# Kernel optimization log

Hardware: AMD Instinct MI355X
Metric: run time of the kernel (lower is better)

Reference implementation:

```python
import jax, jax.numpy as jnp
import numpy as np

FONT_NUM = 190
HID = 256
HEADS = 2
EPS = 1e-5


def _bn(x, g, b, m, v):
    # eval-mode BatchNorm over the last (channel) axis
    return (x - m) * (g * jax.lax.rsqrt(v + EPS)) + b


def _gru(x, Wih, Whh, bih, bhh):
    # x: [B, S, D]; PyTorch gate order r, z, n. Returns all hidden states [B, S, H].
    B, S, _ = x.shape
    H = Whh.shape[1]
    xp = x @ Wih.T + bih  # [B, S, 3H] -- one big GEMM for all timesteps
    def step(h, xt):
        gh = h @ Whh.T + bhh
        xr, xz, xn = jnp.split(xt, 3, axis=-1)
        hr, hz, hn = jnp.split(gh, 3, axis=-1)
        r = jax.nn.sigmoid(xr + hr)
        z = jax.nn.sigmoid(xz + hz)
        n = jnp.tanh(xn + r * hn)
        h_new = (1.0 - z) * n + z * h
        return h_new, h_new
    h0 = jnp.zeros((B, H), x.dtype)
    _, hs = jax.lax.scan(step, h0, jnp.swapaxes(xp, 0, 1))
    return jnp.swapaxes(hs, 0, 1)


def _forward(img_emb, text_embs, len_mask, label_mask, labels,
             img_W, img_b, img_g, img_beta, img_m, img_v,
             g1_Wih, g1_Whh, g1_bih, g1_bhh, tl_W, tl_b,
             t_g, t_beta, t_m, t_v,
             g2_Wih, g2_Whh, g2_bih, g2_bhh, cl_W, cl_b,
             c_g, c_beta, c_m, c_v,
             attn_Win, attn_bin, attn_Wout, attn_bout, pred_W, pred_b):
    # img encoder: Linear -> BN -> (Dropout eval=id) -> ReLU
    img_fea = jax.nn.relu(_bn(img_emb @ img_W.T + img_b, img_g, img_beta, img_m, img_v))  # [B,H]
    # text encoder: GRU -> ReLU -> Linear, then BN+ReLU (torch does this in [B,C,S]; equivalent over channels)
    t = jax.nn.relu(_gru(text_embs, g1_Wih, g1_Whh, g1_bih, g1_bhh))
    t = t @ tl_W.T + tl_b
    text_fea = jax.nn.relu(_bn(t, t_g, t_beta, t_m, t_v))  # [B,S,H]
    len_info = len_mask.sum(axis=1)  # [B]
    # NOTE: sum over ALL timesteps divided by valid length (faithful to source)
    mean = text_fea.sum(axis=1) / len_info[:, None]  # [B,H]
    contrast = text_fea - mean[:, None, :]
    c = jax.nn.relu(_gru(contrast, g2_Wih, g2_Whh, g2_bih, g2_bhh))
    c = c @ cl_W.T + cl_b
    contrast_fea = jax.nn.relu(_bn(c, c_g, c_beta, c_m, c_v))  # [B,S,H]
    B, S, H = text_fea.shape
    hd = H // HEADS
    # batched 3-token self-attention: collapse the per-timestep python loop into one call
    tokens = jnp.stack([
        jnp.broadcast_to(img_fea[:, None, :], (B, S, H)), text_fea, contrast_fea
    ], axis=0).reshape(3, B * S, H)  # [3, N, H]
    Wq, Wk, Wv = jnp.split(attn_Win, 3, axis=0)
    bq, bk, bv = jnp.split(attn_bin, 3, axis=0)
    scale = 1.0 / jnp.sqrt(jnp.asarray(hd, tokens.dtype))
    q = (tokens @ Wq.T + bq).reshape(3, B * S, HEADS, hd) * scale
    k = (tokens @ Wk.T + bk).reshape(3, B * S, HEADS, hd)
    v = (tokens @ Wv.T + bv).reshape(3, B * S, HEADS, hd)
    scores = jnp.einsum('tnhd,snhd->nhts', q, k)  # [N, heads, 3, 3]
    attn = jax.nn.softmax(scores, axis=-1)
    o = jnp.einsum('nhts,snhd->tnhd', attn, v).reshape(3, B * S, H)
    o = o @ attn_Wout.T + attn_bout
    last = o.mean(axis=0).reshape(B, S, H)  # att_fea.mean(0) over the 3 tokens
    logits = last @ pred_W.T + pred_b  # [B,S,FONT_NUM]
    pred = jax.nn.softmax(logits, axis=-1)
    oh = jnp.maximum(label_mask, jax.nn.one_hot(labels, FONT_NUM, dtype=pred.dtype))
    loss = -(oh * jnp.log(pred)).sum(axis=-1)  # [B,S]
    loss = (loss * len_mask).sum(axis=1) / len_info
    return loss.mean()


def setup_inputs() -> dict:
    key = jax.random.key(0)
    ks = jax.random.split(key, 16)
    B, S, D, H = 128, 128, 2048, HID
    img_emb = jax.random.normal(ks[0], (B, D), jnp.float32)
    text_embs = jax.random.normal(ks[1], (B, S, D), jnp.float32)
    lengths = jax.random.randint(ks[2], (B,), S // 2, S + 1)
    len_mask = (jnp.arange(S)[None, :] < lengths[:, None]).astype(jnp.float32)
    labels = jax.random.randint(ks[3], (B, S), 0, FONT_NUM)
    label_mask = jnp.zeros((B, S, FONT_NUM), jnp.float32)
    w = lambda k, sh: jax.random.normal(k, sh, jnp.float32) * 0.02
    params = dict(
        img_W=w(ks[4], (H, D)), img_b=jnp.zeros((H,)),
        img_g=jnp.ones((H,)), img_beta=jnp.zeros((H,)), img_m=jnp.zeros((H,)), img_v=jnp.ones((H,)),
        g1_Wih=w(ks[5], (3 * (H // 2), D)), g1_Whh=w(ks[6], (3 * (H // 2), H // 2)),
        g1_bih=jnp.zeros((3 * (H // 2),)), g1_bhh=jnp.zeros((3 * (H // 2),)),
        tl_W=w(ks[7], (H, H // 2)), tl_b=jnp.zeros((H,)),
        t_g=jnp.ones((H,)), t_beta=jnp.zeros((H,)), t_m=jnp.zeros((H,)), t_v=jnp.ones((H,)),
        g2_Wih=w(ks[8], (3 * H, H)), g2_Whh=w(ks[9], (3 * H, H)),
        g2_bih=jnp.zeros((3 * H,)), g2_bhh=jnp.zeros((3 * H,)),
        cl_W=w(ks[10], (H, H)), cl_b=jnp.zeros((H,)),
        c_g=jnp.ones((H,)), c_beta=jnp.zeros((H,)), c_m=jnp.zeros((H,)), c_v=jnp.ones((H,)),
        attn_Win=w(ks[11], (3 * H, H)), attn_bin=jnp.zeros((3 * H,)),
        attn_Wout=w(ks[12], (H, H)), attn_bout=jnp.zeros((H,)),
        pred_W=w(ks[13], (FONT_NUM, H)), pred_b=jnp.zeros((FONT_NUM,)),
    )
    return dict(img_emb=img_emb, text_embs=text_embs, len_mask=len_mask,
                label_mask=label_mask, labels=labels, **params)


def reference(img_emb, text_embs, len_mask, label_mask, labels,
              img_W, img_b, img_g, img_beta, img_m, img_v,
              g1_Wih, g1_Whh, g1_bih, g1_bhh, tl_W, tl_b,
              t_g, t_beta, t_m, t_v,
              g2_Wih, g2_Whh, g2_bih, g2_bhh, cl_W, cl_b,
              c_g, c_beta, c_m, c_v,
              attn_Win, attn_bin, attn_Wout, attn_bout, pred_W, pred_b):
    return _forward(img_emb, text_embs, len_mask, label_mask, labels,
                    img_W, img_b, img_g, img_beta, img_m, img_v,
                    g1_Wih, g1_Whh, g1_bih, g1_bhh, tl_W, tl_b,
                    t_g, t_beta, t_m, t_v,
                    g2_Wih, g2_Whh, g2_bih, g2_bhh, cl_W, cl_b,
                    c_g, c_beta, c_m, c_v,
                    attn_Win, attn_bin, attn_Wout, attn_bout, pred_W, pred_b)
```

## Files before the change

### kernel.cpp

```cpp
#include <hip/hip_runtime.h>

typedef __attribute__((ext_vector_type(8))) short short8;
typedef __attribute__((ext_vector_type(4))) float f32x4;
typedef _Float16 f16;
typedef __attribute__((ext_vector_type(2))) _Float16 f16x2;
typedef __attribute__((ext_vector_type(8))) _Float16 f16x8;

__device__ inline float bf2f(unsigned short u){
  union{float f; unsigned u32;} x; x.u32 = ((unsigned)u) << 16; return x.f;
}
__device__ inline unsigned short f2bf(float f){
  union{float f; unsigned u;} x; x.f = f;
  unsigned r = (x.u + 0x7FFFu + ((x.u >> 16) & 1u)) >> 16;
  return (unsigned short)r;
}

#if defined(__has_builtin)
#  if __has_builtin(__builtin_amdgcn_fdot2)
#    define HAS_FDOT2 1
#  endif
#endif
__device__ inline float dot2f(f16x2 a, f16x2 b, float c){
#ifdef HAS_FDOT2
  return __builtin_amdgcn_fdot2(a, b, c, false);
#else
  return c + (float)a.x * (float)b.x + (float)a.y * (float)b.y;
#endif
}
__device__ inline f16x2 asf16x2(int v){ return __builtin_bit_cast(f16x2, v); }
__device__ inline int pack2(float lo, float hi){
  f16x2 p = f16x2{(f16)lo, (f16)hi};
  return __builtin_bit_cast(int, p);
}

__device__ inline float sigmoidf_(float x){ return 1.f / (1.f + __expf(-x)); }
__device__ inline float tanh_fast(float x){ float e = __expf(2.f * x); return 1.f - 2.f / (e + 1.f); }

__device__ inline float dpp_xor1(float x){
  return __int_as_float(__builtin_amdgcn_update_dpp(0, __float_as_int(x), 0xB1, 0xF, 0xF, true));
}
__device__ inline float dpp_xor2(float x){
  return __int_as_float(__builtin_amdgcn_update_dpp(0, __float_as_int(x), 0x4E, 0xF, 0xF, true));
}

__device__ inline void load8bf(const unsigned short* p, float* o){
  uint4 q = *(const uint4*)p;
  o[0]=bf2f((unsigned short)(q.x & 0xffffu)); o[1]=bf2f((unsigned short)(q.x >> 16));
  o[2]=bf2f((unsigned short)(q.y & 0xffffu)); o[3]=bf2f((unsigned short)(q.y >> 16));
  o[4]=bf2f((unsigned short)(q.z & 0xffffu)); o[5]=bf2f((unsigned short)(q.z >> 16));
  o[6]=bf2f((unsigned short)(q.w & 0xffffu)); o[7]=bf2f((unsigned short)(q.w >> 16));
}

#define GLL16(g, l) __builtin_amdgcn_global_load_lds(                      \
    (const __attribute__((address_space(1))) void*)(g),                    \
    (__attribute__((address_space(3))) void*)(l), 16, 0, 0)

__global__ __launch_bounds__(256) void conv_all_k(
    const float* __restrict__ s0, const float* __restrict__ s1,
    const float* __restrict__ s2, const float* __restrict__ s3,
    const float* __restrict__ s4, const float* __restrict__ s5,
    const float* __restrict__ s6, const float* __restrict__ s7,
    unsigned short* __restrict__ d0, unsigned short* __restrict__ d1,
    unsigned short* __restrict__ d2, f16* __restrict__ d3,
    unsigned short* __restrict__ d4, unsigned short* __restrict__ d5,
    unsigned short* __restrict__ d6, unsigned short* __restrict__ d7)
{
  int i = blockIdx.x * 256 + threadIdx.x;
  if (i >= 516096) return;
  const float* src; int local; int mode = 0; unsigned short* dst = nullptr; f16* dstf = nullptr;
  if (i < 196608)      { src = s0; local = i;           dst = d0; }
  else if (i < 204800) { src = s1; local = i - 196608;  dst = d1; }
  else if (i < 253952) { src = s2; local = i - 204800;  dst = d2; }
  else if (i < 303104) { src = s3; local = i - 253952;  dstf = d3; mode = 1; }
  else if (i < 319488) { src = s4; local = i - 303104;  dst = d4; }
  else if (i < 368640) { src = s5; local = i - 319488;  dst = d5; }
  else if (i < 385024) { src = s6; local = i - 368640;  dst = d6; }
  else                 { src = s7; local = i - 385024;  dst = d7; }
  float4 v = ((const float4*)src)[local];
  if (mode == 0) {
    union { unsigned short s[4]; uint2 q; } u;
    u.s[0]=f2bf(v.x); u.s[1]=f2bf(v.y); u.s[2]=f2bf(v.z); u.s[3]=f2bf(v.w);
    ((uint2*)dst)[local] = u.q;
  } else {
    union { f16 s[4]; uint2 q; } u;
    u.s[0]=(f16)v.x; u.s[1]=(f16)v.y; u.s[2]=(f16)v.z; u.s[3]=(f16)v.w;
    ((uint2*)dstf)[local] = u.q;
  }
}

__global__ __launch_bounds__(256) void pred_pad_k(const float* __restrict__ W,
                                                  const float* __restrict__ b,
                                                  unsigned short* __restrict__ Wd,
                                                  float* __restrict__ bd){
  int i = blockIdx.x * 256 + threadIdx.x;
  int j = i >> 8;
  Wd[i] = (j < 190) ? f2bf(W[i]) : (unsigned short)0;
  if (i < 192) bd[i] = (i < 190) ? b[i] : 0.f;
}

template<int OUT_T, bool BN, int A_MODE, bool MEAN_OUT>
__global__ __launch_bounds__(256) void gemm128_k(
    const void* __restrict__ Ap, const unsigned short* __restrict__ Bw,
    const float* __restrict__ bias,
    const float* __restrict__ gam, const float* __restrict__ bet,
    const float* __restrict__ mu,  const float* __restrict__ var,
    void* __restrict__ Cp, int M, int N, int K,
    const float* __restrict__ lmask, float* __restrict__ mean_out,
    float* __restrict__ len_out)
{
  __shared__ __align__(16) unsigned short As[4096];
  __shared__ __align__(16) unsigned short Bs[4096];
  __shared__ float msh[2][128];
  __shared__ float lsum[128];
  __shared__ float lenshv;
  const int tid  = threadIdx.x;
  const int lane = tid & 63, wid = tid >> 6;
  const int wm = wid & 1, wn = wid >> 1;
  const int bm = blockIdx.y << 7, bn = blockIdx.x << 7;
  const int rA = tid >> 2, seg = tid & 3;

  if (MEAN_OUT) {
    if (tid < 128) lsum[tid] = lmask[(size_t)(bm >> 7) * 128 + tid];
    __syncthreads();
    if (tid < 64) lsum[tid] += lsum[tid + 64];
    __syncthreads();
    if (tid == 0) { float s = 0.f; for (int i = 0; i < 64; i++) s += lsum[i]; lenshv = s; }
    __syncthreads();
  }

  f32x4 acc[4][4];
  #pragma unroll
  for (int i = 0; i < 4; i++)
    #pragma unroll
    for (int j = 0; j < 4; j++)
      acc[i][j] = f32x4{0.f, 0.f, 0.f, 0.f};

  const unsigned short* Abf = (const unsigned short*)Ap;
  const float* Af = (const float*)Ap;
  char* asb = (char*)As;
  char* bsb = (char*)Bs;
  char* asw = asb + wid * 1024;
  char* bsw = bsb + wid * 1024;

  for (int k0 = 0; k0 < K; k0 += 32) {
    if (A_MODE == 1) {
      #pragma unroll
      for (int beta = 0; beta < 2; beta++) {
        const float* src = Af + (size_t)(bm + rA + beta * 64) * K + k0 + seg * 8;
        float4 v0 = *(const float4*)src;
        float4 v1 = *(const float4*)(src + 4);
        union { unsigned short s[8]; uint4 q; } u;
        u.s[0]=f2bf(v0.x); u.s[1]=f2bf(v0.y); u.s[2]=f2bf(v0.z); u.s[3]=f2bf(v0.w);
        u.s[4]=f2bf(v1.x); u.s[5]=f2bf(v1.y); u.s[6]=f2bf(v1.z); u.s[7]=f2bf(v1.w);
        *(uint4*)(asb + beta * 4096 + tid * 16) = u.q;
      }
    } else if (A_MODE == 2) {
      const float* mrow = mu + (size_t)(bm >> 7) * 256 + k0 + seg * 8;
      float4 m0 = *(const float4*)mrow;
      float4 m1 = *(const float4*)(mrow + 4);
      #pragma unroll
      for (int beta = 0; beta < 2; beta++) {
        const unsigned short* src = Abf + (size_t)(bm + rA + beta * 64) * K + k0 + seg * 8;
        float av[8];
        load8bf(src, av);
        union { unsigned short s[8]; uint4 q; } u;
        u.s[0]=f2bf(av[0]-m0.x); u.s[1]=f2bf(av[1]-m0.y); u.s[2]=f2bf(av[2]-m0.z); u.s[3]=f2bf(av[3]-m0.w);
        u.s[4]=f2bf(av[4]-m1.x); u.s[5]=f2bf(av[5]-m1.y); u.s[6]=f2bf(av[6]-m1.z); u.s[7]=f2bf(av[7]-m1.w);
        *(uint4*)(asb + beta * 4096 + tid * 16) = u.q;
      }
    } else {
      GLL16(Abf + (size_t)(bm + rA)      * K + k0 + seg * 8, asw);
      GLL16(Abf + (size_t)(bm + rA + 64) * K + k0 + seg * 8, asw + 4096);
    }
    GLL16(Bw + (size_t)(bn + rA)      * K + k0 + seg * 8, bsw);
    GLL16(Bw + (size_t)(bn + rA + 64) * K + k0 + seg * 8, bsw + 4096);
    __syncthreads();

    short8 a[4], b[4];
    #pragma unroll
    for (int f = 0; f < 4; f++) {
      int ra = wm * 64 + f * 16 + (lane & 15);
      a[f] = *(const short8*)(asb + ra * 64 + (lane >> 4) * 16);
      int rb = wn * 64 + f * 16 + (lane & 15);
      b[f] = *(const short8*)(bsb + rb * 64 + (lane >> 4) * 16);
    }
    #pragma unroll
    for (int fm = 0; fm < 4; fm++)
      #pragma unroll
      for (int fn = 0; fn < 4; fn++)
        acc[fm][fn] = __builtin_amdgcn_mfma_f32_16x16x32_bf16(a[fm], b[fn], acc[fm][fn], 0, 0, 0);
    __syncthreads();
  }

  #pragma unroll
  for (int fn = 0; fn < 4; fn++) {
    int col = bn + wn * 64 + fn * 16 + (lane & 15);
    float bs = bias[col];
    float sc = 1.f, sh = 0.f;
    if (BN) { float s = gam[col] * rsqrtf(var[col] + 1e-5f); sc = s; sh = bet[col] - mu[col] * s; }
    float colacc = 0.f;
    #pragma unroll
    for (int fm = 0; fm < 4; fm++) {
      int row = bm + wm * 64 + fm * 16 + ((lane >> 4) << 2);
      #pragma unroll
      for (int j = 0; j < 4; j++) {
        float v = acc[fm][fn][j] + bs;
        if (BN) { v = v * sc + sh; v = fmaxf(v, 0.f); }
        size_t idx = (size_t)(row + j) * N + col;
        if (OUT_T == 1) ((f16*)Cp)[idx] = (f16)v;
        else            ((unsigned short*)Cp)[idx] = f2bf(v);
        if (MEAN_OUT) colacc += v;
      }
    }
    if (MEAN_OUT) {
      colacc += __shfl_xor(colacc, 16);
      colacc += __shfl_xor(colacc, 32);
      if ((lane >> 4) == 0) msh[wm][wn * 64 + fn * 16 + lane] = colacc;
    }
  }
  if (MEAN_OUT) {
    __syncthreads();
    if (tid < 128) {
      float tot = msh[0][tid] + msh[1][tid];
      mean_out[(size_t)(bm >> 7) * 256 + bn + tid] = tot / lenshv;
    }
    if (bn == 0 && tid == 0) len_out[bm >> 7] = lenshv;
  }
}

__global__ __launch_bounds__(256) void gemmqkv_k(
    const unsigned short* __restrict__ tfea, const unsigned short* __restrict__ cfea,
    const unsigned short* __restrict__ imgf, const unsigned short* __restrict__ Bw,
    const float* __restrict__ bias,
    unsigned short* __restrict__ q1, unsigned short* __restrict__ q2,
    unsigned short* __restrict__ q0)
{
  const int N = 768, K = 256;
  __shared__ __align__(16) unsigned short As[4096];
  __shared__ __align__(16) unsigned short Bs[4096];
  const int tid  = threadIdx.x;
  const int lane = tid & 63, wid = tid >> 6;
  const int wm = wid & 1, wn = wid >> 1;
  const int y = blockIdx.y;
  const unsigned short* Abf; unsigned short* Cp; int bm;
  if (y < 128)      { Abf = tfea; Cp = q1; bm = y << 7; }
  else if (y < 256) { Abf = cfea; Cp = q2; bm = (y - 128) << 7; }
  else              { Abf = imgf; Cp = q0; bm = 0; }
  const int bn = blockIdx.x << 7;
  const int rA = tid >> 2, seg = tid & 3;

  f32x4 acc[4][4];
  #pragma unroll
  for (int i = 0; i < 4; i++)
    #pragma unroll
    for (int j = 0; j < 4; j++)
      acc[i][j] = f32x4{0.f, 0.f, 0.f, 0.f};

  char* asb = (char*)As;
  char* bsb = (char*)Bs;
  char* asw = asb + wid * 1024;
  char* bsw = bsb + wid * 1024;

  for (int k0 = 0; k0 < K; k0 += 32) {
    GLL16(Abf + (size_t)(bm + rA)      * K + k0 + seg * 8, asw);
    GLL16(Abf + (size_t)(bm + rA + 64) * K + k0 + seg * 8, asw + 4096);
    GLL16(Bw + (size_t)(bn + rA)      * K + k0 + seg * 8, bsw);
    GLL16(Bw + (size_t)(bn + rA + 64) * K + k0 + seg * 8, bsw + 4096);
    __syncthreads();

    short8 a[4], b[4];
    #pragma unroll
    for (int f = 0; f < 4; f++) {
      int ra = wm * 64 + f * 16 + (lane & 15);
      a[f] = *(const short8*)(asb + ra * 64 + (lane >> 4) * 16);
      int rb = wn * 64 + f * 16 + (lane & 15);
      b[f] = *(const short8*)(bsb + rb * 64 + (lane >> 4) * 16);
    }
    #pragma unroll
    for (int fm = 0; fm < 4; fm++)
      #pragma unroll
      for (int fn = 0; fn < 4; fn++)
        acc[fm][fn] = __builtin_amdgcn_mfma_f32_16x16x32_bf16(a[fm], b[fn], acc[fm][fn], 0, 0, 0);
    __syncthreads();
  }

  #pragma unroll
  for (int fn = 0; fn < 4; fn++) {
    int col = bn + wn * 64 + fn * 16 + (lane & 15);
    float bs = bias[col];
    #pragma unroll
    for (int fm = 0; fm < 4; fm++) {
      int row = bm + wm * 64 + fm * 16 + ((lane >> 4) << 2);
      #pragma unroll
      for (int j = 0; j < 4; j++) {
        float v = acc[fm][fn][j] + bs;
        Cp[(size_t)(row + j) * N + col] = f2bf(v);
      }
    }
  }
}

template<int OUT_T, bool BN, bool AF32>
__global__ __launch_bounds__(256) void gemm_k(
    const void* __restrict__ Ap, const unsigned short* __restrict__ Bw,
    const float* __restrict__ bias,
    const float* __restrict__ gam, const float* __restrict__ bet,
    const float* __restrict__ mu,  const float* __restrict__ var,
    void* __restrict__ Cp, int M, int N, int K)
{
  __shared__ unsigned short As[64][40];
  __shared__ unsigned short Bs[64][40];
  const int tid  = threadIdx.x;
  const int lane = tid & 63, wid = tid >> 6;
  const int wm = wid & 1, wn = wid >> 1;
  const int bm = blockIdx.y << 6, bn = blockIdx.x << 6;
  const int srow = tid >> 2, sseg = tid & 3;

  f32x4 acc[2][2];
  #pragma unroll
  for (int i = 0; i < 2; i++)
    #pragma unroll
    for (int j = 0; j < 2; j++)
      acc[i][j] = f32x4{0.f, 0.f, 0.f, 0.f};

  const unsigned short* Abf = (const unsigned short*)Ap;
  const float* Af = (const float*)Ap;

  for (int k0 = 0; k0 < K; k0 += 32) {
    if (AF32) {
      const float* src = Af + (size_t)(bm + srow) * K + k0 + sseg * 8;
      float4 v0 = *(const float4*)(src);
      float4 v1 = *(const float4*)(src + 4);
      union { unsigned short s[8]; uint4 q; } u;
      u.s[0]=f2bf(v0.x); u.s[1]=f2bf(v0.y); u.s[2]=f2bf(v0.z); u.s[3]=f2bf(v0.w);
      u.s[4]=f2bf(v1.x); u.s[5]=f2bf(v1.y); u.s[6]=f2bf(v1.z); u.s[7]=f2bf(v1.w);
      *(uint4*)&As[srow][sseg * 8] = u.q;
    } else {
      *(uint4*)&As[srow][sseg * 8] =
          *(const uint4*)(Abf + (size_t)(bm + srow) * K + k0 + sseg * 8);
    }
    *(uint4*)&Bs[srow][sseg * 8] =
        *(const uint4*)(Bw + (size_t)(bn + srow) * K + k0 + sseg * 8);
    __syncthreads();

    short8 a0 = *(const short8*)&As[wm * 32 +      (lane & 15)][(lane >> 4) * 8];
    short8 a1 = *(const short8*)&As[wm * 32 + 16 + (lane & 15)][(lane >> 4) * 8];
    short8 b0 = *(const short8*)&Bs[wn * 32 +      (lane & 15)][(lane >> 4) * 8];
    short8 b1 = *(const short8*)&Bs[wn * 32 + 16 + (lane & 15)][(lane >> 4) * 8];
    acc[0][0] = __builtin_amdgcn_mfma_f32_16x16x32_bf16(a0, b0, acc[0][0], 0, 0, 0);
    acc[0][1] = __builtin_amdgcn_mfma_f32_16x16x32_bf16(a0, b1, acc[0][1], 0, 0, 0);
    acc[1][0] = __builtin_amdgcn_mfma_f32_16x16x32_bf16(a1, b0, acc[1][0], 0, 0, 0);
    acc[1][1] = __builtin_amdgcn_mfma_f32_16x16x32_bf16(a1, b1, acc[1][1], 0, 0, 0);
    __syncthreads();
  }

  #pragma unroll
  for (int fn = 0; fn < 2; fn++) {
    int col = bn + wn * 32 + fn * 16 + (lane & 15);
    float bs = bias[col];
    float sc = 1.f, sh = 0.f;
    if (BN) { float s = gam[col] * rsqrtf(var[col] + 1e-5f); sc = s; sh = bet[col] - mu[col] * s; }
    #pragma unroll
    for (int fm = 0; fm < 2; fm++) {
      int row = bm + wm * 32 + fm * 16 + ((lane >> 4) << 2);
      #pragma unroll
      for (int j = 0; j < 4; j++) {
        float v = acc[fm][fn][j] + bs;
        if (BN) { v = v * sc + sh; v = fmaxf(v, 0.f); }
        size_t idx = (size_t)(row + j) * N + col;
        if (OUT_T == 0)      ((float*)Cp)[idx] = v;
        else if (OUT_T == 1) ((f16*)Cp)[idx]   = (f16)v;
        else                 ((unsigned short*)Cp)[idx] = f2bf(v);
      }
    }
  }
}

__global__ __launch_bounds__(512, 2) void gru2_scan_k(
    const f16* __restrict__ Wf,
    const float* __restrict__ bhh,
    const f16* __restrict__ xp, unsigned short* __restrict__ hs_relu)
{
  const int b = blockIdx.x;
  const int tid = threadIdx.x;
  const int jj = tid >> 1, kh = tid & 1;
  __shared__ __align__(16) f16 hbuf[2][256];

  int wri[64], wzi[64];
  #pragma unroll
  for (int i = 0; i < 16; i++) {
    const int kb = kh * 128 + i * 8;
    uint4 q;
    q = *(const uint4*)&Wf[(size_t)(jj      ) * 256 + kb];
    wri[4*i+0] = (int)q.x; wri[4*i+1] = (int)q.y; wri[4*i+2] = (int)q.z; wri[4*i+3] = (int)q.w;
    q = *(const uint4*)&Wf[(size_t)(jj + 256) * 256 + kb];
    wzi[4*i+0] = (int)q.x; wzi[4*i+1] = (int)q.y; wzi[4*i+2] = (int)q.z; wzi[4*i+3] = (int)q.w;
  }
  #pragma unroll
  for (int i = 0; i < 64; i++)
    asm volatile("" : "+v"(wri[i]), "+v"(wzi[i]));

  const f16* nsrc = Wf + (size_t)(512 + jj) * 256 + kh * 128;

  const float br = bhh[jj], bz = bhh[jj + 256], bn2 = bhh[jj + 512];
  if (tid < 256) hbuf[0][tid] = (f16)0.f;
  float hprev = 0.f;
  f16 pxr = (f16)0.f, pxz = (f16)0.f, pxn = (f16)0.f;
  if (kh == 0) {
    const f16* x0 = xp + (size_t)(b * 128) * 768;
    pxr = x0[jj]; pxz = x0[256 + jj]; pxn = x0[512 + jj];
  }
  __syncthreads();
  int cur = 0;
  for (int t = 0; t < 128; t++) {
    float xr = (float)pxr, xz = (float)pxz, xn = (float)pxn;
    if (kh == 0) {
      const int tn = (t < 127) ? (t + 1) : 127;
      const f16* xnr = xp + (size_t)(b * 128 + tn) * 768;
      pxr = xnr[jj]; pxz = xnr[256 + jj]; pxn = xnr[512 + jj];
    }
    uint4 nb[4];
    #pragma unroll
    for (int c = 0; c < 4; c++) nb[c] = *(const uint4*)(nsrc + c * 8);

    const char* hb = (const char*)hbuf[cur] + kh * 256;
    float ar = 0.f, az = 0.f, an = 0.f;
    #pragma unroll
    for (int i = 0; i < 16; i++) {
      f16x8 hv = *(const f16x8*)(hb + i * 16);
      f16x8 nv = __builtin_bit_cast(f16x8, nb[i & 3]);
      if (i < 12) nb[i & 3] = *(const uint4*)(nsrc + (i + 4) * 8);
      #pragma unroll
      for (int u = 0; u < 4; u++) {
        f16x2 hp = f16x2{hv[2*u], hv[2*u+1]};
        ar = dot2f(asf16x2(wri[4*i+u]), hp, ar);
        az = dot2f(asf16x2(wzi[4*i+u]), hp, az);
        an = dot2f(f16x2{nv[2*u], nv[2*u+1]}, hp, an);
      }
    }
    ar += dpp_xor1(ar);
    az += dpp_xor1(az);
    an += dpp_xor1(an);
    if (kh == 0) {
      float r = sigmoidf_(xr + ar + br);
      float z = sigmoidf_(xz + az + bz);
      float n = tanh_fast(xn + r * (an + bn2));
      float hnew = (1.f - z) * n + z * hprev;
      hprev = hnew;
      hbuf[cur ^ 1][jj] = (f16)hnew;
      hs_relu[(size_t)(b * 128 + t) * 256 + jj] = f2bf(fmaxf(hnew, 0.f));
    }
    __syncthreads();
    cur ^= 1;
  }
}

__global__ __launch_bounds__(512, 4) void gru1_scan_k(
    const float* __restrict__ Whh, const float* __restrict__ bhh,
    const f16* __restrict__ xp, unsigned short* __restrict__ hs_relu)
{
  const int b = blockIdx.x;
  const int tid = threadIdx.x;
  const int jj = tid >> 2, kh = tid & 3;
  __shared__ __align__(16) f16 hbuf[2][128];

  int wri[16], wzi[16], wni[16];
  #pragma unroll
  for (int i = 0; i < 4; i++) {
    const int kb = kh * 32 + i * 8;
    float4 f0, f1;
    f0 = *(const float4*)&Whh[(size_t)(jj      ) * 128 + kb];
    f1 = *(const float4*)&Whh[(size_t)(jj      ) * 128 + kb + 4];
    wri[4*i+0] = pack2(f0.x, f0.y); wri[4*i+1] = pack2(f0.z, f0.w);
    wri[4*i+2] = pack2(f1.x, f1.y); wri[4*i+3] = pack2(f1.z, f1.w);
    f0 = *(const float4*)&Whh[(size_t)(jj + 128) * 128 + kb];
    f1 = *(const float4*)&Whh[(size_t)(jj + 128) * 128 + kb + 4];
    wzi[4*i+0] = pack2(f0.x, f0.y); wzi[4*i+1] = pack2(f0.z, f0.w);
    wzi[4*i+2] = pack2(f1.x, f1.y); wzi[4*i+3] = pack2(f1.z, f1.w);
    f0 = *(const float4*)&Whh[(size_t)(jj + 256) * 128 + kb];
    f1 = *(const float4*)&Whh[(size_t)(jj + 256) * 128 + kb + 4];
    wni[4*i+0] = pack2(f0.x, f0.y); wni[4*i+1] = pack2(f0.z, f0.w);
    wni[4*i+2] = pack2(f1.x, f1.y); wni[4*i+3] = pack2(f1.z, f1.w);
  }
  #pragma unroll
  for (int i = 0; i < 16; i++)
    asm volatile("" : "+v"(wri[i]), "+v"(wzi[i]), "+v"(wni[i]));

  const float br = bhh[jj], bz = bhh[jj + 128], bn2 = bhh[jj + 256];
  if (tid < 128) hbuf[0][tid] = (f16)0.f;
  float hprev = 0.f;
  f16 pxr = (f16)0.f, pxz = (f16)0.f, pxn = (f16)0.f;
  if (kh == 0) {
    const f16* x0 = xp + (size_t)(b * 128) * 384;
    pxr = x0[jj]; pxz = x0[128 + jj]; pxn = x0[256 + jj];
  }
  __syncthreads();
  int cur = 0;
  for (int t = 0; t < 128; t++) {
    float xr = (float)pxr, xz = (float)pxz, xn = (float)pxn;
    if (kh == 0) {
      const int tn = (t < 127) ? (t + 1) : 127;
      const f16* xnr = xp + (size_t)(b * 128 + tn) * 384;
      pxr = xnr[jj]; pxz = xnr[128 + jj]; pxn = xnr[256 + jj];
    }
    const char* hb = (const char*)hbuf[cur] + kh * 64;
    float ar = 0.f, az = 0.f, an = 0.f;
    #pragma unroll
    for (int c = 0; c < 4; c++) {
      f16x8 hv = *(const f16x8*)(hb + c * 16);
      #pragma unroll
      for (int u = 0; u < 4; u++) {
        f16x2 hp = f16x2{hv[2*u], hv[2*u+1]};
        ar = dot2f(asf16x2(wri[4*c+u]), hp, ar);
        az = dot2f(asf16x2(wzi[4*c+u]), hp, az);
        an = dot2f(asf16x2(wni[4*c+u]), hp, an);
      }
    }
    ar += dpp_xor1(ar); ar += dpp_xor2(ar);
    az += dpp_xor1(az); az += dpp_xor2(az);
    an += dpp_xor1(an); an += dpp_xor2(an);
    if (kh == 0) {
      float r = sigmoidf_(xr + ar + br);
      float z = sigmoidf_(xz + az + bz);
      float n = tanh_fast(xn + r * (an + bn2));
      float hnew = (1.f - z) * n + z * hprev;
      hprev = hnew;
      hbuf[cur ^ 1][jj] = (f16)hnew;
      hs_relu[(size_t)(b * 128 + t) * 128 + jj] = f2bf(fmaxf(hnew, 0.f));
    }
    __syncthreads();
    cur ^= 1;
  }
}

__global__ __launch_bounds__(256) void attn_k(const unsigned short* __restrict__ qkv0,
                                              const unsigned short* __restrict__ qkv1,
                                              const unsigned short* __restrict__ qkv2,
                                              unsigned short* __restrict__ osum){
  int i = blockIdx.x * 256 + threadIdx.x;
  int h = i & 1; int n = i >> 1; int b = n >> 7;
  const unsigned short* t0 = qkv0 + (size_t)b * 768 + h * 128;
  const unsigned short* t1 = qkv1 + (size_t)n * 768 + h * 128;
  const unsigned short* t2 = qkv2 + (size_t)n * 768 + h * 128;
  float sc[3][3];
  #pragma unroll
  for (int a = 0; a < 3; a++)
    #pragma unroll
    for (int s = 0; s < 3; s++) sc[a][s] = 0.f;
  #pragma unroll 1
  for (int dc = 0; dc < 16; dc++) {
    float q[3][8], k[3][8];
    load8bf(t0 + dc * 8, q[0]); load8bf(t1 + dc * 8, q[1]); load8bf(t2 + dc * 8, q[2]);
    load8bf(t0 + 256 + dc * 8, k[0]); load8bf(t1 + 256 + dc * 8, k[1]); load8bf(t2 + 256 + dc * 8, k[2]);
    #pragma unroll
    for (int a = 0; a < 3; a++)
      #pragma unroll
      for (int s = 0; s < 3; s++) {
        float d = 0.f;
        #pragma unroll
        for (int e = 0; e < 8; e++) d += q[a][e] * k[s][e];
        sc[a][s] += d;
      }
  }
  const float scale = 0.08838834764831845f;
  float w[3] = {0.f, 0.f, 0.f};
  #pragma unroll
  for (int a = 0; a < 3; a++) {
    float s0 = sc[a][0] * scale, s1 = sc[a][1] * scale, s2 = sc[a][2] * scale;
    float m = fmaxf(s0, fmaxf(s1, s2));
    float e0 = __expf(s0 - m), e1 = __expf(s1 - m), e2 = __expf(s2 - m);
    float inv = 1.f / (e0 + e1 + e2);
    w[0] += e0 * inv; w[1] += e1 * inv; w[2] += e2 * inv;
  }
  w[0] *= (1.f / 3.f); w[1] *= (1.f / 3.f); w[2] *= (1.f / 3.f);
  unsigned short* op = osum + (size_t)n * 256 + h * 128;
  #pragma unroll 1
  for (int dc = 0; dc < 16; dc++) {
    float v0[8], v1[8], v2[8];
    load8bf(t0 + 512 + dc * 8, v0); load8bf(t1 + 512 + dc * 8, v1); load8bf(t2 + 512 + dc * 8, v2);
    union { unsigned short s[8]; uint4 q; } u;
    #pragma unroll
    for (int e = 0; e < 8; e++) u.s[e] = f2bf(w[0] * v0[e] + w[1] * v1[e] + w[2] * v2[e]);
    *(uint4*)(op + dc * 8) = u.q;
  }
}

__global__ __launch_bounds__(64) void loss_k(const float* __restrict__ logits,
                                             const float* __restrict__ label_mask,
                                             const int* __restrict__ labels,
                                             float* __restrict__ loss_raw){
  int r = blockIdx.x; int j = threadIdx.x;
  int lab = labels[r];
  float l[3]; float m = -1e30f;
  #pragma unroll
  for (int q = 0; q < 3; q++) {
    int c = j + q * 64;
    float lv = (c < 190) ? logits[(size_t)r * 192 + c] : -1e30f;
    l[q] = lv; m = fmaxf(m, lv);
  }
  #pragma unroll
  for (int off = 32; off; off >>= 1) m = fmaxf(m, __shfl_xor(m, off));
  float se = 0.f, soh = 0.f, dot = 0.f;
  #pragma unroll
  for (int q = 0; q < 3; q++) {
    int c = j + q * 64;
    if (c < 190) {
      se += expf(l[q] - m);
      float oh = fmaxf(label_mask[(size_t)r * 190 + c], (c == lab) ? 1.f : 0.f);
      soh += oh; dot += oh * l[q];
    }
  }
  #pragma unroll
  for (int off = 32; off; off >>= 1) {
    se += __shfl_xor(se, off); soh += __shfl_xor(soh, off); dot += __shfl_xor(dot, off);
  }
  if (j == 0) loss_raw[r] = (m + logf(se)) * soh - dot;
}

__global__ __launch_bounds__(256) void final_k(const float* __restrict__ loss_raw,
                                               const float* __restrict__ len_mask,
                                               const float* __restrict__ len_info,
                                               float* __restrict__ out){
  __shared__ float sh[256];
  int t = threadIdx.x;
  float acc = 0.f;
  for (int i = t; i < 16384; i += 256) acc += loss_raw[i] * len_mask[i] / len_info[i >> 7];
  sh[t] = acc; __syncthreads();
  for (int s = 128; s; s >>= 1) { if (t < s) sh[t] += sh[t + s]; __syncthreads(); }
  if (t == 0) out[0] = sh[0] / 128.f;
}

extern "C" void kernel_launch(void* const* d_in, const int* in_sizes, int n_in,
                              void* d_out, int out_size, void* d_ws, size_t ws_size,
                              hipStream_t stream)
{
  const float* img_emb    = (const float*)d_in[0];
  const float* text_embs  = (const float*)d_in[1];
  const float* len_mask   = (const float*)d_in[2];
  const float* label_mask = (const float*)d_in[3];
  const int*   labels     = (const int*)  d_in[4];
  const float* img_W   = (const float*)d_in[5];
  const float* img_b   = (const float*)d_in[6];
  const float* img_g   = (const float*)d_in[7];
  const float* img_be  = (const float*)d_in[8];
  const float* img_m   = (const float*)d_in[9];
  const float* img_v   = (const float*)d_in[10];
  const float* g1_Wih  = (const float*)d_in[11];
  const float* g1_Whh  = (const float*)d_in[12];
  const float* g1_bih  = (const float*)d_in[13];
  const float* g1_bhh  = (const float*)d_in[14];
  const float* tl_W    = (const float*)d_in[15];
  const float* tl_b    = (const float*)d_in[16];
  const float* t_g     = (const float*)d_in[17];
  const float* t_be    = (const float*)d_in[18];
  const float* t_m     = (const float*)d_in[19];
  const float* t_v     = (const float*)d_in[20];
  const float* g2_Wih  = (const float*)d_in[21];
  const float* g2_Whh  = (const float*)d_in[22];
  const float* g2_bih  = (const float*)d_in[23];
  const float* g2_bhh  = (const float*)d_in[24];
  const float* cl_W    = (const float*)d_in[25];
  const float* cl_b    = (const float*)d_in[26];
  const float* c_g     = (const float*)d_in[27];
  const float* c_be    = (const float*)d_in[28];
  const float* c_m     = (const float*)d_in[29];
  const float* c_v     = (const float*)d_in[30];
  const float* a_Win   = (const float*)d_in[31];
  const float* a_bin   = (const float*)d_in[32];
  const float* a_Wout  = (const float*)d_in[33];
  const float* a_bout  = (const float*)d_in[34];
  const float* pred_W  = (const float*)d_in[35];
  const float* pred_b  = (const float*)d_in[36];

  char* ws = (char*)d_ws;
  size_t o = 0;
  auto alloc = [&](size_t sz){ size_t r = o; o += (sz + 255) & ~(size_t)255; return r; };

  size_t o_g1Wih = alloc(384ull*2048*2);
  size_t o_tlW   = alloc(256ull*128*2);
  size_t o_g2Wih = alloc(768ull*256*2);
  size_t o_g2Whh = alloc(768ull*256*2);
  size_t o_clW   = alloc(256ull*256*2);
  size_t o_aWin  = alloc(768ull*256*2);
  size_t o_aWout = alloc(256ull*256*2);
  size_t o_imgW  = alloc(256ull*2048*2);
  size_t o_predW = alloc(192ull*256*2);
  size_t o_predb = alloc(192ull*4);
  size_t o_imgfea= alloc(128ull*256*2);
  size_t o_mean  = alloc(128ull*256*4);
  size_t o_len   = alloc(128ull*4);
  size_t o_R0    = alloc(33554432ull);
  size_t o_RB    = alloc(25165824ull);
  size_t o_tfea  = alloc(16384ull*256*2);
  size_t o_qkv1  = alloc(16384ull*768*2);
  size_t o_cfea  = alloc(16384ull*256*2);
  size_t o_qkv0  = alloc(128ull*768*2);
  size_t o_loss  = alloc(16384ull*4);
  (void)ws_size; (void)in_sizes; (void)n_in; (void)out_size;

  unsigned short* g1Wih_bf = (unsigned short*)(ws + o_g1Wih);
  unsigned short* tlW_bf   = (unsigned short*)(ws + o_tlW);
  unsigned short* g2Wih_bf = (unsigned short*)(ws + o_g2Wih);
  f16*            g2Whh_f  = (f16*)(ws + o_g2Whh);
  unsigned short* clW_bf   = (unsigned short*)(ws + o_clW);
  unsigned short* aWin_bf  = (unsigned short*)(ws + o_aWin);
  unsigned short* aWout_bf = (unsigned short*)(ws + o_aWout);
  unsigned short* imgW_bf  = (unsigned short*)(ws + o_imgW);
  unsigned short* predW_bf = (unsigned short*)(ws + o_predW);
  float*          predb_p  = (float*)(ws + o_predb);
  unsigned short* img_fea  = (unsigned short*)(ws + o_imgfea);
  float*          meanb    = (float*)(ws + o_mean);
  float*          len_info = (float*)(ws + o_len);
  f16*            xp2      = (f16*)(ws + o_R0);
  unsigned short* hs2      = (unsigned short*)(ws + o_R0 + 25165824ull);
  unsigned short* osum     = (unsigned short*)(ws + o_R0);
  unsigned short* lastb    = (unsigned short*)(ws + o_R0 + 8388608ull);
  f16*            xp1      = (f16*)(ws + o_RB);
  unsigned short* hs1      = (unsigned short*)(ws + o_RB + 12582912ull);
  unsigned short* qkv2     = (unsigned short*)(ws + o_RB);
  unsigned short* tfea     = (unsigned short*)(ws + o_tfea);
  unsigned short* qkv1     = (unsigned short*)(ws + o_qkv1);
  float*          logits   = (float*)(ws + o_qkv1);
  unsigned short* cfea     = (unsigned short*)(ws + o_cfea);
  unsigned short* qkv0     = (unsigned short*)(ws + o_qkv0);
  float*          loss_raw = (float*)(ws + o_loss);
  float*          outp     = (float*)d_out;

  conv_all_k<<<2016, 256, 0, stream>>>(
      g1_Wih, tl_W, g2_Wih, g2_Whh, cl_W, a_Win, a_Wout, img_W,
      g1Wih_bf, tlW_bf, g2Wih_bf, g2Whh_f, clW_bf, aWin_bf, aWout_bf, imgW_bf);
  pred_pad_k<<<192, 256, 0, stream>>>(pred_W, pred_b, predW_bf, predb_p);

  gemm128_k<2, true, 1, false><<<dim3(2, 1), 256, 0, stream>>>(
      img_emb, imgW_bf, img_b, img_g, img_be, img_m, img_v, img_fea, 128, 256, 2048,
      nullptr, nullptr, nullptr);

  gemm128_k<1, false, 1, false><<<dim3(3, 128), 256, 0, stream>>>(
      text_embs, g1Wih_bf, g1_bih, nullptr, nullptr, nullptr, nullptr, xp1, 16384, 384, 2048,
      nullptr, nullptr, nullptr);

  gru1_scan_k<<<128, 512, 0, stream>>>(g1_Whh, g1_bhh, xp1, hs1);

  gemm128_k<2, true, 0, true><<<dim3(2, 128), 256, 0, stream>>>(
      hs1, tlW_bf, tl_b, t_g, t_be, t_m, t_v, tfea, 16384, 256, 128,
      len_mask, meanb, len_info);

  gemm128_k<1, false, 2, false><<<dim3(6, 128), 256, 0, stream>>>(
      tfea, g2Wih_bf, g2_bih, nullptr, nullptr, meanb, nullptr, xp2, 16384, 768, 256,
      nullptr, nullptr, nullptr);

  gru2_scan_k<<<128, 512, 0, stream>>>(g2Whh_f, g2_bhh, xp2, hs2);

  gemm128_k<2, true, 0, false><<<dim3(2, 128), 256, 0, stream>>>(
      hs2, clW_bf, cl_b, c_g, c_be, c_m, c_v, cfea, 16384, 256, 256,
      nullptr, nullptr, nullptr);

  gemmqkv_k<<<dim3(6, 257), 256, 0, stream>>>(
      tfea, cfea, img_fea, aWin_bf, a_bin, qkv1, qkv2, qkv0);

  attn_k<<<128, 256, 0, stream>>>(qkv0, qkv1, qkv2, osum);

  gemm128_k<2, false, 0, false><<<dim3(2, 128), 256, 0, stream>>>(
      osum, aWout_bf, a_bout, nullptr, nullptr, nullptr, nullptr, lastb, 16384, 256, 256,
      nullptr, nullptr, nullptr);

  gemm_k<0, false, false><<<dim3(3, 256), 256, 0, stream>>>(
      lastb, predW_bf, predb_p, nullptr, nullptr, nullptr, nullptr, logits, 16384, 192, 256);

  loss_k<<<16384, 64, 0, stream>>>(logits, label_mask, labels, loss_raw);
  final_k<<<1, 256, 0, stream>>>(loss_raw, len_mask, len_info, outp);
}
```

Measured before the change: 569.3 us.

## Fuse prediction GEMM with cross-entropy loss, keeping logits in LDS

Replaces the pred-head GEMM plus a separate per-row loss kernel with one kernel. Each block loads a 64-row A tile covering the full K=256 once, loops over three 64-column weight chunks, writes logits into shared memory, then computes the softmax-CE loss per row using 4 threads per row and DPP reductions. This removes the fp32 logits round trip through global memory and one launch. In exchange the block uses large LDS (about 114KB), which limits occupancy, and runs serial per-thread loops over 48 columns.

```diff
diff --git a/kernel.cpp b/kernel.cpp
--- a/kernel.cpp
+++ b/kernel.cpp
@@ -300,80 +300,94 @@
   }
 }
 
-template<int OUT_T, bool BN, bool AF32>
-__global__ __launch_bounds__(256) void gemm_k(
-    const void* __restrict__ Ap, const unsigned short* __restrict__ Bw,
+__global__ __launch_bounds__(256) void gemm_loss_k(
+    const unsigned short* __restrict__ A,
+    const unsigned short* __restrict__ Bw,
     const float* __restrict__ bias,
-    const float* __restrict__ gam, const float* __restrict__ bet,
-    const float* __restrict__ mu,  const float* __restrict__ var,
-    void* __restrict__ Cp, int M, int N, int K)
+    const float* __restrict__ label_mask,
+    const int* __restrict__ labels,
+    float* __restrict__ loss_raw)
 {
-  __shared__ unsigned short As[64][40];
-  __shared__ unsigned short Bs[64][40];
+  __shared__ __align__(16) unsigned short As[64 * 256];
+  __shared__ __align__(16) unsigned short Bs[64 * 256];
+  __shared__ float lg[64][196];
   const int tid  = threadIdx.x;
   const int lane = tid & 63, wid = tid >> 6;
   const int wm = wid & 1, wn = wid >> 1;
-  const int bm = blockIdx.y << 6, bn = blockIdx.x << 6;
-  const int srow = tid >> 2, sseg = tid & 3;
-
-  f32x4 acc[2][2];
-  #pragma unroll
-  for (int i = 0; i < 2; i++)
-    #pragma unroll
-    for (int j = 0; j < 2; j++)
-      acc[i][j] = f32x4{0.f, 0.f, 0.f, 0.f};
-
-  const unsigned short* Abf = (const unsigned short*)Ap;
-  const float* Af = (const float*)Ap;
-
-  for (int k0 = 0; k0 < K; k0 += 32) {
-    if (AF32) {
-      const float* src = Af + (size_t)(bm + srow) * K + k0 + sseg * 8;
-      float4 v0 = *(const float4*)(src);
-      float4 v1 = *(const float4*)(src + 4);
-      union { unsigned short s[8]; uint4 q; } u;
-      u.s[0]=f2bf(v0.x); u.s[1]=f2bf(v0.y); u.s[2]=f2bf(v0.z); u.s[3]=f2bf(v0.w);
-      u.s[4]=f2bf(v1.x); u.s[5]=f2bf(v1.y); u.s[6]=f2bf(v1.z); u.s[7]=f2bf(v1.w);
-      *(uint4*)&As[srow][sseg * 8] = u.q;
-    } else {
-      *(uint4*)&As[srow][sseg * 8] =
-          *(const uint4*)(Abf + (size_t)(bm + srow) * K + k0 + sseg * 8);
-    }
-    *(uint4*)&Bs[srow][sseg * 8] =
-        *(const uint4*)(Bw + (size_t)(bn + srow) * K + k0 + sseg * 8);
-    __syncthreads();
-
-    short8 a0 = *(const short8*)&As[wm * 32 +      (lane & 15)][(lane >> 4) * 8];
-    short8 a1 = *(const short8*)&As[wm * 32 + 16 + (lane & 15)][(lane >> 4) * 8];
-    short8 b0 = *(const short8*)&Bs[wn * 32 +      (lane & 15)][(lane >> 4) * 8];
-    short8 b1 = *(const short8*)&Bs[wn * 32 + 16 + (lane & 15)][(lane >> 4) * 8];
-    acc[0][0] = __builtin_amdgcn_mfma_f32_16x16x32_bf16(a0, b0, acc[0][0], 0, 0, 0);
-    acc[0][1] = __builtin_amdgcn_mfma_f32_16x16x32_bf16(a0, b1, acc[0][1], 0, 0, 0);
-    acc[1][0] = __builtin_amdgcn_mfma_f32_16x16x32_bf16(a1, b0, acc[1][0], 0, 0, 0);
-    acc[1][1] = __builtin_amdgcn_mfma_f32_16x16x32_bf16(a1, b1, acc[1][1], 0, 0, 0);
-    __syncthreads();
-  }
-
-  #pragma unroll
-  for (int fn = 0; fn < 2; fn++) {
-    int col = bn + wn * 32 + fn * 16 + (lane & 15);
-    float bs = bias[col];
-    float sc = 1.f, sh = 0.f;
-    if (BN) { float s = gam[col] * rsqrtf(var[col] + 1e-5f); sc = s; sh = bet[col] - mu[col] * s; }
-    #pragma unroll
-    for (int fm = 0; fm < 2; fm++) {
-      int row = bm + wm * 32 + fm * 16 + ((lane >> 4) << 2);
-      #pragma unroll
-      for (int j = 0; j < 4; j++) {
-        float v = acc[fm][fn][j] + bs;
-        if (BN) { v = v * sc + sh; v = fmaxf(v, 0.f); }
-        size_t idx = (size_t)(row + j) * N + col;
-        if (OUT_T == 0)      ((float*)Cp)[idx] = v;
-        else if (OUT_T == 1) ((f16*)Cp)[idx]   = (f16)v;
-        else                 ((unsigned short*)Cp)[idx] = f2bf(v);
+  const int bm = blockIdx.x << 6;
+  char* asb = (char*)As;
+  char* bsb = (char*)Bs;
+
+  #pragma unroll
+  for (int p = 0; p < 8; p++)
+    GLL16(A + (size_t)(bm + p * 8 + (tid >> 5)) * 256 + (tid & 31) * 8,
+          asb + p * 4096 + wid * 1024);
+
+  for (int cn = 0; cn < 3; cn++) {
+    #pragma unroll
+    for (int p = 0; p < 8; p++)
+      GLL16(Bw + (size_t)(cn * 64 + p * 8 + (tid >> 5)) * 256 + (tid & 31) * 8,
+            bsb + p * 4096 + wid * 1024);
+    __syncthreads();
+
+    f32x4 acc[2][2];
+    #pragma unroll
+    for (int i = 0; i < 2; i++)
+      #pragma unroll
+      for (int j = 0; j < 2; j++)
+        acc[i][j] = f32x4{0.f, 0.f, 0.f, 0.f};
+
+    #pragma unroll
+    for (int ks = 0; ks < 8; ks++) {
+      short8 a0 = *(const short8*)(asb + (wm * 32 +      (lane & 15)) * 512 + ks * 64 + (lane >> 4) * 16);
+      short8 a1 = *(const short8*)(asb + (wm * 32 + 16 + (lane & 15)) * 512 + ks * 64 + (lane >> 4) * 16);
+      short8 b0 = *(const short8*)(bsb + (wn * 32 +      (lane & 15)) * 512 + ks * 64 + (lane >> 4) * 16);
+      short8 b1 = *(const short8*)(bsb + (wn * 32 + 16 + (lane & 15)) * 512 + ks * 64 + (lane >> 4) * 16);
+      acc[0][0] = __builtin_amdgcn_mfma_f32_16x16x32_bf16(a0, b0, acc[0][0], 0, 0, 0);
+      acc[0][1] = __builtin_amdgcn_mfma_f32_16x16x32_bf16(a0, b1, acc[0][1], 0, 0, 0);
+      acc[1][0] = __builtin_amdgcn_mfma_f32_16x16x32_bf16(a1, b0, acc[1][0], 0, 0, 0);
+      acc[1][1] = __builtin_amdgcn_mfma_f32_16x16x32_bf16(a1, b1, acc[1][1], 0, 0, 0);
+    }
+
+    #pragma unroll
+    for (int fn = 0; fn < 2; fn++) {
+      int col = cn * 64 + wn * 32 + fn * 16 + (lane & 15);
+      float bs = bias[col];
+      #pragma unroll
+      for (int fm = 0; fm < 2; fm++) {
+        int rl = wm * 32 + fm * 16 + ((lane >> 4) << 2);
+        #pragma unroll
+        for (int j = 0; j < 4; j++)
+          lg[rl + j][col] = acc[fm][fn][j] + bs;
       }
     }
-  }
+    __syncthreads();
+  }
+
+  const int r = tid >> 2, q = tid & 3;
+  const int row = bm + r;
+  const int lab = labels[row];
+  float m = -1e30f;
+  #pragma unroll 1
+  for (int c = q * 48; c < q * 48 + 48; c++)
+    if (c < 190) m = fmaxf(m, lg[r][c]);
+  m = fmaxf(m, dpp_xor1(m));
+  m = fmaxf(m, dpp_xor2(m));
+  float se = 0.f, soh = 0.f, dot = 0.f;
+  const float* lmrow = label_mask + (size_t)row * 190;
+  #pragma unroll 1
+  for (int c = q * 48; c < q * 48 + 48; c++) {
+    if (c < 190) {
+      float lv = lg[r][c];
+      se += __expf(lv - m);
+      float oh = fmaxf(lmrow[c], (c == lab) ? 1.f : 0.f);
+      soh += oh; dot += oh * lv;
+    }
+  }
+  se  += dpp_xor1(se);  se  += dpp_xor2(se);
+  soh += dpp_xor1(soh); soh += dpp_xor2(soh);
+  dot += dpp_xor1(dot); dot += dpp_xor2(dot);
+  if (q == 0) loss_raw[row] = (m + __logf(se)) * soh - dot;
 }
 
 __global__ __launch_bounds__(512, 2) void gru2_scan_k(
@@ -583,38 +597,6 @@
     for (int e = 0; e < 8; e++) u.s[e] = f2bf(w[0] * v0[e] + w[1] * v1[e] + w[2] * v2[e]);
     *(uint4*)(op + dc * 8) = u.q;
   }
-}
-
-__global__ __launch_bounds__(64) void loss_k(const float* __restrict__ logits,
-                                             const float* __restrict__ label_mask,
-                                             const int* __restrict__ labels,
-                                             float* __restrict__ loss_raw){
-  int r = blockIdx.x; int j = threadIdx.x;
-  int lab = labels[r];
-  float l[3]; float m = -1e30f;
-  #pragma unroll
-  for (int q = 0; q < 3; q++) {
-    int c = j + q * 64;
-    float lv = (c < 190) ? logits[(size_t)r * 192 + c] : -1e30f;
-    l[q] = lv; m = fmaxf(m, lv);
-  }
-  #pragma unroll
-  for (int off = 32; off; off >>= 1) m = fmaxf(m, __shfl_xor(m, off));
-  float se = 0.f, soh = 0.f, dot = 0.f;
-  #pragma unroll
-  for (int q = 0; q < 3; q++) {
-    int c = j + q * 64;
-    if (c < 190) {
-      se += expf(l[q] - m);
-      float oh = fmaxf(label_mask[(size_t)r * 190 + c], (c == lab) ? 1.f : 0.f);
-      soh += oh; dot += oh * l[q];
-    }
-  }
-  #pragma unroll
-  for (int off = 32; off; off >>= 1) {
-    se += __shfl_xor(se, off); soh += __shfl_xor(soh, off); dot += __shfl_xor(dot, off);
-  }
-  if (j == 0) loss_raw[r] = (m + logf(se)) * soh - dot;
 }
 
 __global__ __launch_bounds__(256) void final_k(const float* __restrict__ loss_raw,
@@ -720,7 +702,6 @@
   unsigned short* qkv2     = (unsigned short*)(ws + o_RB);
   unsigned short* tfea     = (unsigned short*)(ws + o_tfea);
   unsigned short* qkv1     = (unsigned short*)(ws + o_qkv1);
-  float*          logits   = (float*)(ws + o_qkv1);
   unsigned short* cfea     = (unsigned short*)(ws + o_cfea);
   unsigned short* qkv0     = (unsigned short*)(ws + o_qkv0);
   float*          loss_raw = (float*)(ws + o_loss);
@@ -764,9 +745,8 @@
       osum, aWout_bf, a_bout, nullptr, nullptr, nullptr, nullptr, lastb, 16384, 256, 256,
       nullptr, nullptr, nullptr);
 
-  gemm_k<0, false, false><<<dim3(3, 256), 256, 0, stream>>>(
-      lastb, predW_bf, predb_p, nullptr, nullptr, nullptr, nullptr, logits, 16384, 192, 256);
-
-  loss_k<<<16384, 64, 0, stream>>>(logits, label_mask, labels, loss_raw);
+  gemm_loss_k<<<256, 256, 0, stream>>>(
+      lastb, predW_bf, predb_p, label_mask, labels, loss_raw);
+
   final_k<<<1, 256, 0, stream>>>(loss_raw, len_mask, len_info, outp);
 }
```

Measured after the change: 574.8 us. Within noise of the previous version (+1.0%).
